# Kernel optimization log

Measured on AMD Instinct MI355X. Metric: run time of the kernel, lower is better.

## Reference

```python
import jax, jax.numpy as jnp
import numpy as np
import math

N_NODES = 100000
N_PAIRS = 640000
F_TOTAL = 128
N_HEADS = 8
HEAD_DIM = F_TOTAL // N_HEADS  # 16


def setup_inputs() -> dict:
    key = jax.random.key(0)
    ks = jax.random.split(key, 8)
    x = jax.random.normal(ks[0], (N_NODES, F_TOTAL), dtype=jnp.float32)
    w_ij = jax.random.normal(ks[1], (N_PAIRS, F_TOTAL), dtype=jnp.float32)
    idx_i = jax.random.randint(ks[2], (N_PAIRS,), 0, N_NODES, dtype=jnp.int32)
    idx_j = jax.random.randint(ks[3], (N_PAIRS,), 0, N_NODES, dtype=jnp.int32)
    phi_r_cut = jax.random.uniform(ks[4], (N_PAIRS,), dtype=jnp.float32)
    # per-head linear weights, nn.Linear convention: y = x @ W.T, W: (out, in)
    s = 1.0 / math.sqrt(HEAD_DIM)
    wq = jax.random.uniform(ks[5], (N_HEADS, HEAD_DIM, HEAD_DIM), jnp.float32, -s, s)
    wk = jax.random.uniform(ks[6], (N_HEADS, HEAD_DIM, HEAD_DIM), jnp.float32, -s, s)
    wv = jax.random.uniform(ks[7], (N_HEADS, HEAD_DIM, HEAD_DIM), jnp.float32, -s, s)
    return {"x": x, "w_ij": w_ij, "idx_i": idx_i, "idx_j": idx_j,
            "phi_r_cut": phi_r_cut, "wq": wq, "wk": wk, "wv": wv}


def reference(x, w_ij, idx_i, idx_j, phi_r_cut, wq, wk, wv):
    n, f = x.shape
    h, d = wq.shape[0], wq.shape[1]
    # split into heads: (H, n, d) and (H, P, d)
    xh = x.reshape(n, h, d).transpose(1, 0, 2)
    wh = w_ij.reshape(-1, h, d).transpose(1, 0, 2)
    # per-head linear projections (y = x @ W.T)
    q = jnp.einsum('hnd,hed->hne', xh, wq)  # (H, n, d)
    k = jnp.einsum('hnd,hed->hne', xh, wk)
    v = jnp.einsum('hnd,hed->hne', xh, wv)
    # filter-modulated dot-product attention coefficients per pair
    alpha = (q[:, idx_i] * wh * k[:, idx_j]).sum(-1) / math.sqrt(d)  # (H, P)
    alpha = alpha * phi_r_cut[None, :]
    # message + scatter-add aggregation
    msg = alpha[..., None] * v[:, idx_j]  # (H, P, d)
    y = jax.vmap(lambda m: jax.ops.segment_sum(m, idx_i, num_segments=n))(msg)  # (H, n, d)
    return y.transpose(1, 0, 2).reshape(n, f)
```

## Files before the change

### kernel.cpp

```cpp
#include <hip/hip_runtime.h>
#include <hip/hip_fp16.h>

#define F_TOTAL 128
#define N_HEADS 8
#define HEAD_DIM 16
#define SCAN_ITEMS 1024

typedef float vf4 __attribute__((ext_vector_type(4)));
typedef int   vi4 __attribute__((ext_vector_type(4)));

__global__ __launch_bounds__(256) void proj_hist_kernel(
    const float* __restrict__ x,
    const float* __restrict__ wq,
    const float* __restrict__ wk,
    const float* __restrict__ wv,
    const int*   __restrict__ idx_i,
    float* __restrict__ q, __half2* __restrict__ kv,
    int*   __restrict__ hist,
    int n_nodes, int n_pairs)
{
    const int gid = blockIdx.x * 256 + threadIdx.x;
    const int stride = gridDim.x * 256;
    const int f = gid & (F_TOTAL - 1);

    float rq[16], rk[16], rv[16];
    const float4* wq4 = (const float4*)wq;
    const float4* wk4 = (const float4*)wk;
    const float4* wv4 = (const float4*)wv;
    #pragma unroll
    for (int d4 = 0; d4 < 4; ++d4) {
        float4 a = wq4[f * 4 + d4];
        rq[d4*4+0]=a.x; rq[d4*4+1]=a.y; rq[d4*4+2]=a.z; rq[d4*4+3]=a.w;
        float4 b = wk4[f * 4 + d4];
        rk[d4*4+0]=b.x; rk[d4*4+1]=b.y; rk[d4*4+2]=b.z; rk[d4*4+3]=b.w;
        float4 c = wv4[f * 4 + d4];
        rv[d4*4+0]=c.x; rv[d4*4+1]=c.y; rv[d4*4+2]=c.z; rv[d4*4+3]=c.w;
    }
    const int lanebase = (f & 112) & 63;

    const int total = n_nodes * F_TOTAL;
    for (int idx = gid; idx < total; idx += stride) {
        const float xval = __builtin_nontemporal_load(x + idx);
        float aq = 0.f, ak = 0.f, av = 0.f;
        #pragma unroll
        for (int d = 0; d < 16; ++d) {
            const float xv = __shfl(xval, lanebase + d);
            aq += xv * rq[d];
            ak += xv * rk[d];
            av += xv * rv[d];
        }
        q[idx] = aq;
        kv[idx] = __floats2half2_rn(ak, av);
    }

    for (int p = gid; p < n_pairs; p += stride)
        atomicAdd(&hist[idx_i[p]], 1);
}

__global__ __launch_bounds__(256) void scan_reduce_kernel(
    const int* __restrict__ hist, int* __restrict__ blockSums, int n)
{
    __shared__ int ls[256];
    const int t = threadIdx.x;
    const int base = blockIdx.x * SCAN_ITEMS + t * 4;
    int s = 0;
    if (base + 3 < n) {
        int4 h = *(const int4*)(hist + base);
        s = h.x + h.y + h.z + h.w;
    } else {
        for (int kk = 0; kk < 4; ++kk)
            if (base + kk < n) s += hist[base + kk];
    }
    ls[t] = s;
    __syncthreads();
    for (int off = 128; off > 0; off >>= 1) {
        if (t < off) ls[t] += ls[t + off];
        __syncthreads();
    }
    if (t == 0) blockSums[blockIdx.x] = ls[0];
}

__global__ __launch_bounds__(256) void scan_apply_kernel(
    const int* __restrict__ hist, const int* __restrict__ blockSums,
    int* __restrict__ offsets, int n, int nblk)
{
    __shared__ int ls[256];
    const int t = threadIdx.x;
    const int bid = blockIdx.x;

    int s = 0;
    for (int b = t; b < bid; b += 256) s += blockSums[b];
    ls[t] = s;
    __syncthreads();
    for (int off = 128; off > 0; off >>= 1) {
        if (t < off) ls[t] += ls[t + off];
        __syncthreads();
    }
    const int base0 = ls[0];
    __syncthreads();

    const int base = bid * SCAN_ITEMS + t * 4;
    int h0 = 0, h1 = 0, h2 = 0, h3 = 0;
    if (base + 3 < n) {
        int4 h = *(const int4*)(hist + base);
        h0 = h.x; h1 = h.y; h2 = h.z; h3 = h.w;
    } else {
        if (base + 0 < n) h0 = hist[base + 0];
        if (base + 1 < n) h1 = hist[base + 1];
        if (base + 2 < n) h2 = hist[base + 2];
        if (base + 3 < n) h3 = hist[base + 3];
    }
    const int tsum = h0 + h1 + h2 + h3;
    ls[t] = tsum;
    __syncthreads();
    for (int off = 1; off < 256; off <<= 1) {
        int add = (t >= off) ? ls[t - off] : 0;
        __syncthreads();
        ls[t] += add;
        __syncthreads();
    }
    int off = base0 + (ls[t] - tsum);
    if (base + 0 < n) offsets[base + 0] = off; off += h0;
    if (base + 1 < n) offsets[base + 1] = off; off += h1;
    if (base + 2 < n) offsets[base + 2] = off; off += h2;
    if (base + 3 < n) offsets[base + 3] = off;
}

__global__ __launch_bounds__(256) void scatter_kernel(
    const int* __restrict__ idx_i, const int* __restrict__ idx_j,
    const float* __restrict__ phi,
    int* __restrict__ offsets,
    vi4* __restrict__ meta,
    int n_pairs)
{
    const int p = blockIdx.x * 256 + threadIdx.x;
    if (p < n_pairs) {
        const int i = idx_i[p];
        const int pos = atomicAdd(&offsets[i], 1);
        meta[pos] = (vi4){p, idx_j[p], __float_as_int(phi[p]), 0};
    }
}

__global__ __launch_bounds__(256) void segment_kernel(
    const float* __restrict__ q,
    const __half2* __restrict__ kv,
    const float* __restrict__ w_ij,
    const int* __restrict__ hist,
    const int* __restrict__ offsets,
    const vi4* __restrict__ meta,
    float* __restrict__ out,
    int n_nodes)
{
    const int node = blockIdx.x * 4 + (threadIdx.x >> 6);
    if (node >= n_nodes) return;
    const int lane = threadIdx.x & 63;
    const int half = lane >> 5;
    const int t    = lane & 31;

    const int cnt   = hist[node];
    const int start = offsets[node] - cnt;
    const vf4 q4 = *((const vf4*)(q + (size_t)node * F_TOTAL) + t);

    vf4 acc = (vf4){0.f, 0.f, 0.f, 0.f};

    const int my0 = start + half;
    const int rem = (cnt > half) ? ((cnt - half + 1) >> 1) : 0;

    union HU { vi4 i; __half2 h[4]; };

    if (rem > 0) {
        vi4 m0 = meta[my0];
        vi4 m1 = meta[my0 + 2];
        int r = 0;
        for (; r + 2 <= rem; r += 2) {
            const vi4 n0 = meta[my0 + 2 * (r + 2)];
            const vi4 n1 = meta[my0 + 2 * (r + 3)];
            const vf4 wA = __builtin_nontemporal_load(
                (const vf4*)(w_ij + (size_t)m0.x * F_TOTAL) + t);
            HU A; A.i = *((const vi4*)kv + (size_t)m0.y * 32 + t);
            const vf4 wB = __builtin_nontemporal_load(
                (const vf4*)(w_ij + (size_t)m1.x * F_TOTAL) + t);
            HU B; B.i = *((const vi4*)kv + (size_t)m1.y * 32 + t);

            const float2 a0 = __half22float2(A.h[0]);
            const float2 a1 = __half22float2(A.h[1]);
            const float2 a2 = __half22float2(A.h[2]);
            const float2 a3 = __half22float2(A.h[3]);
            const float2 b0 = __half22float2(B.h[0]);
            const float2 b1 = __half22float2(B.h[1]);
            const float2 b2 = __half22float2(B.h[2]);
            const float2 b3 = __half22float2(B.h[3]);

            float sA = q4.x*wA.x*a0.x + q4.y*wA.y*a1.x + q4.z*wA.z*a2.x + q4.w*wA.w*a3.x;
            float sB = q4.x*wB.x*b0.x + q4.y*wB.y*b1.x + q4.z*wB.z*b2.x + q4.w*wB.w*b3.x;
            sA += __shfl_xor(sA, 1); sA += __shfl_xor(sA, 2);
            sB += __shfl_xor(sB, 1); sB += __shfl_xor(sB, 2);
            const float alA = sA * 0.25f * __int_as_float(m0.z);
            const float alB = sB * 0.25f * __int_as_float(m1.z);
            acc.x += alA * a0.y; acc.y += alA * a1.y;
            acc.z += alA * a2.y; acc.w += alA * a3.y;
            acc.x += alB * b0.y; acc.y += alB * b1.y;
            acc.z += alB * b2.y; acc.w += alB * b3.y;
            m0 = n0; m1 = n1;
        }
        if (r < rem) {
            const vf4 wA = __builtin_nontemporal_load(
                (const vf4*)(w_ij + (size_t)m0.x * F_TOTAL) + t);
            HU A; A.i = *((const vi4*)kv + (size_t)m0.y * 32 + t);
            const float2 a0 = __half22float2(A.h[0]);
            const float2 a1 = __half22float2(A.h[1]);
            const float2 a2 = __half22float2(A.h[2]);
            const float2 a3 = __half22float2(A.h[3]);
            float sA = q4.x*wA.x*a0.x + q4.y*wA.y*a1.x + q4.z*wA.z*a2.x + q4.w*wA.w*a3.x;
            sA += __shfl_xor(sA, 1); sA += __shfl_xor(sA, 2);
            const float alA = sA * 0.25f * __int_as_float(m0.z);
            acc.x += alA * a0.y; acc.y += alA * a1.y;
            acc.z += alA * a2.y; acc.w += alA * a3.y;
        }
    }

    acc.x += __shfl_xor(acc.x, 32);
    acc.y += __shfl_xor(acc.y, 32);
    acc.z += __shfl_xor(acc.z, 32);
    acc.w += __shfl_xor(acc.w, 32);
    if (half == 0)
        __builtin_nontemporal_store(acc, (vf4*)(out + (size_t)node * F_TOTAL) + t);
}

extern "C" void kernel_launch(void* const* d_in, const int* in_sizes, int n_in,
                              void* d_out, int out_size, void* d_ws, size_t ws_size,
                              hipStream_t stream)
{
    const float* x     = (const float*)d_in[0];
    const float* w_ij  = (const float*)d_in[1];
    const int*   idx_i = (const int*)d_in[2];
    const int*   idx_j = (const int*)d_in[3];
    const float* phi   = (const float*)d_in[4];
    const float* wq    = (const float*)d_in[5];
    const float* wk    = (const float*)d_in[6];
    const float* wv    = (const float*)d_in[7];

    const int n_nodes = in_sizes[0] / F_TOTAL;
    const int n_pairs = in_sizes[2];
    const size_t node_elems = (size_t)n_nodes * F_TOTAL;

    float*   q         = (float*)d_ws;
    __half2* kv        = (__half2*)(q + node_elems);
    vi4*     meta      = (vi4*)((char*)kv + node_elems * sizeof(__half2));
    int*     hist      = (int*)(meta + n_pairs + 8);
    int*     offsets   = hist + n_nodes;
    int*     blockSums = offsets + n_nodes;

    hipMemsetAsync(hist, 0, (size_t)n_nodes * sizeof(int), stream);

    proj_hist_kernel<<<3072, 256, 0, stream>>>(
        x, wq, wk, wv, idx_i, q, kv, hist, n_nodes, n_pairs);

    const int nblk = (n_nodes + SCAN_ITEMS - 1) / SCAN_ITEMS;
    scan_reduce_kernel<<<nblk, 256, 0, stream>>>(hist, blockSums, n_nodes);
    scan_apply_kernel<<<nblk, 256, 0, stream>>>(hist, blockSums, offsets,
                                                n_nodes, nblk);

    const int pair_blocks = (n_pairs + 255) / 256;
    scatter_kernel<<<pair_blocks, 256, 0, stream>>>(
        idx_i, idx_j, phi, offsets, meta, n_pairs);

    segment_kernel<<<(n_nodes + 3) / 4, 256, 0, stream>>>(
        q, kv, w_ij, hist, offsets, meta, (float*)d_out, n_nodes);
}
```

Measured before the change: 590.8 us.

## Pre-sort w_ij into destination order as fp16 during scatter

```diff
diff --git a/kernel.cpp b/kernel.cpp
--- a/kernel.cpp
+++ b/kernel.cpp
@@ -129,25 +129,43 @@
 __global__ __launch_bounds__(256) void scatter_kernel(
     const int* __restrict__ idx_i, const int* __restrict__ idx_j,
     const float* __restrict__ phi,
+    const float* __restrict__ w_ij,
     int* __restrict__ offsets,
-    vi4* __restrict__ meta,
+    int2* __restrict__ meta,
+    __half* __restrict__ w16s,
     int n_pairs)
 {
-    const int p = blockIdx.x * 256 + threadIdx.x;
-    if (p < n_pairs) {
-        const int i = idx_i[p];
-        const int pos = atomicAdd(&offsets[i], 1);
-        meta[pos] = (vi4){p, idx_j[p], __float_as_int(phi[p]), 0};
-    }
+    const int grp = (blockIdx.x * 256 + threadIdx.x) >> 4;
+    const int l16 = threadIdx.x & 15;
+    const int lane = threadIdx.x & 63;
+    if (grp >= n_pairs) return;
+
+    int pos = 0;
+    if (l16 == 0) pos = atomicAdd(&offsets[idx_i[grp]], 1);
+    pos = __shfl(pos, lane & 48);
+
+    const vf4 wa = __builtin_nontemporal_load(
+        (const vf4*)(w_ij + (size_t)grp * F_TOTAL) + l16 * 2);
+    const vf4 wb = __builtin_nontemporal_load(
+        (const vf4*)(w_ij + (size_t)grp * F_TOTAL) + l16 * 2 + 1);
+    union { vi4 i; __half2 h[4]; } o;
+    o.h[0] = __floats2half2_rn(wa.x, wa.y);
+    o.h[1] = __floats2half2_rn(wa.z, wa.w);
+    o.h[2] = __floats2half2_rn(wb.x, wb.y);
+    o.h[3] = __floats2half2_rn(wb.z, wb.w);
+    *((vi4*)w16s + (size_t)pos * 16 + l16) = o.i;
+
+    if (l16 == 0)
+        meta[pos] = (int2){idx_j[grp], __float_as_int(phi[grp])};
 }
 
 __global__ __launch_bounds__(256) void segment_kernel(
     const float* __restrict__ q,
     const __half2* __restrict__ kv,
-    const float* __restrict__ w_ij,
+    const __half* __restrict__ w16s,
     const int* __restrict__ hist,
     const int* __restrict__ offsets,
-    const vi4* __restrict__ meta,
+    const int2* __restrict__ meta,
     float* __restrict__ out,
     int n_nodes)
 {
@@ -167,21 +185,24 @@
     const int rem = (cnt > half) ? ((cnt - half + 1) >> 1) : 0;
 
     union HU { vi4 i; __half2 h[4]; };
+    union WU { int2 i2; __half2 h[2]; };
 
     if (rem > 0) {
-        vi4 m0 = meta[my0];
-        vi4 m1 = meta[my0 + 2];
+        int2 m0 = meta[my0];
+        int2 m1 = meta[my0 + 2];
         int r = 0;
         for (; r + 2 <= rem; r += 2) {
-            const vi4 n0 = meta[my0 + 2 * (r + 2)];
-            const vi4 n1 = meta[my0 + 2 * (r + 3)];
-            const vf4 wA = __builtin_nontemporal_load(
-                (const vf4*)(w_ij + (size_t)m0.x * F_TOTAL) + t);
-            HU A; A.i = *((const vi4*)kv + (size_t)m0.y * 32 + t);
-            const vf4 wB = __builtin_nontemporal_load(
-                (const vf4*)(w_ij + (size_t)m1.x * F_TOTAL) + t);
-            HU B; B.i = *((const vi4*)kv + (size_t)m1.y * 32 + t);
-
+            const int2 n0 = meta[my0 + 2 * (r + 2)];
+            const int2 n1 = meta[my0 + 2 * (r + 3)];
+            WU wA; wA.i2 = *(const int2*)(w16s + (size_t)(my0 + 2*r)     * F_TOTAL + t * 4);
+            HU A;  A.i   = *((const vi4*)kv + (size_t)m0.x * 32 + t);
+            WU wB; wB.i2 = *(const int2*)(w16s + (size_t)(my0 + 2*(r+1)) * F_TOTAL + t * 4);
+            HU B;  B.i   = *((const vi4*)kv + (size_t)m1.x * 32 + t);
+
+            const float2 wa0 = __half22float2(wA.h[0]);
+            const float2 wa1 = __half22float2(wA.h[1]);
+            const float2 wb0 = __half22float2(wB.h[0]);
+            const float2 wb1 = __half22float2(wB.h[1]);
             const float2 a0 = __half22float2(A.h[0]);
             const float2 a1 = __half22float2(A.h[1]);
             const float2 a2 = __half22float2(A.h[2]);
@@ -191,12 +212,12 @@
             const float2 b2 = __half22float2(B.h[2]);
             const float2 b3 = __half22float2(B.h[3]);
 
-            float sA = q4.x*wA.x*a0.x + q4.y*wA.y*a1.x + q4.z*wA.z*a2.x + q4.w*wA.w*a3.x;
-            float sB = q4.x*wB.x*b0.x + q4.y*wB.y*b1.x + q4.z*wB.z*b2.x + q4.w*wB.w*b3.x;
+            float sA = q4.x*wa0.x*a0.x + q4.y*wa0.y*a1.x + q4.z*wa1.x*a2.x + q4.w*wa1.y*a3.x;
+            float sB = q4.x*wb0.x*b0.x + q4.y*wb0.y*b1.x + q4.z*wb1.x*b2.x + q4.w*wb1.y*b3.x;
             sA += __shfl_xor(sA, 1); sA += __shfl_xor(sA, 2);
             sB += __shfl_xor(sB, 1); sB += __shfl_xor(sB, 2);
-            const float alA = sA * 0.25f * __int_as_float(m0.z);
-            const float alB = sB * 0.25f * __int_as_float(m1.z);
+            const float alA = sA * 0.25f * __int_as_float(m0.y);
+            const float alB = sB * 0.25f * __int_as_float(m1.y);
             acc.x += alA * a0.y; acc.y += alA * a1.y;
             acc.z += alA * a2.y; acc.w += alA * a3.y;
             acc.x += alB * b0.y; acc.y += alB * b1.y;
@@ -204,16 +225,17 @@
             m0 = n0; m1 = n1;
         }
         if (r < rem) {
-            const vf4 wA = __builtin_nontemporal_load(
-                (const vf4*)(w_ij + (size_t)m0.x * F_TOTAL) + t);
-            HU A; A.i = *((const vi4*)kv + (size_t)m0.y * 32 + t);
+            WU wA; wA.i2 = *(const int2*)(w16s + (size_t)(my0 + 2*r) * F_TOTAL + t * 4);
+            HU A;  A.i   = *((const vi4*)kv + (size_t)m0.x * 32 + t);
+            const float2 wa0 = __half22float2(wA.h[0]);
+            const float2 wa1 = __half22float2(wA.h[1]);
             const float2 a0 = __half22float2(A.h[0]);
             const float2 a1 = __half22float2(A.h[1]);
             const float2 a2 = __half22float2(A.h[2]);
             const float2 a3 = __half22float2(A.h[3]);
-            float sA = q4.x*wA.x*a0.x + q4.y*wA.y*a1.x + q4.z*wA.z*a2.x + q4.w*wA.w*a3.x;
+            float sA = q4.x*wa0.x*a0.x + q4.y*wa0.y*a1.x + q4.z*wa1.x*a2.x + q4.w*wa1.y*a3.x;
             sA += __shfl_xor(sA, 1); sA += __shfl_xor(sA, 2);
-            const float alA = sA * 0.25f * __int_as_float(m0.z);
+            const float alA = sA * 0.25f * __int_as_float(m0.y);
             acc.x += alA * a0.y; acc.y += alA * a1.y;
             acc.z += alA * a2.y; acc.w += alA * a3.y;
         }
@@ -246,7 +268,8 @@
 
     float*   q         = (float*)d_ws;
     __half2* kv        = (__half2*)(q + node_elems);
-    vi4*     meta      = (vi4*)((char*)kv + node_elems * sizeof(__half2));
+    __half*  w16s      = (__half*)(kv + node_elems);
+    int2*    meta      = (int2*)(w16s + (size_t)(n_pairs + 1) * F_TOTAL);
     int*     hist      = (int*)(meta + n_pairs + 8);
     int*     offsets   = hist + n_nodes;
     int*     blockSums = offsets + n_nodes;
@@ -261,10 +284,10 @@
     scan_apply_kernel<<<nblk, 256, 0, stream>>>(hist, blockSums, offsets,
                                                 n_nodes, nblk);
 
-    const int pair_blocks = (n_pairs + 255) / 256;
-    scatter_kernel<<<pair_blocks, 256, 0, stream>>>(
-        idx_i, idx_j, phi, offsets, meta, n_pairs);
+    const int scat_blocks = (n_pairs * 16 + 255) / 256;
+    scatter_kernel<<<scat_blocks, 256, 0, stream>>>(
+        idx_i, idx_j, phi, w_ij, offsets, meta, w16s, n_pairs);
 
     segment_kernel<<<(n_nodes + 3) / 4, 256, 0, stream>>>(
-        q, kv, w_ij, hist, offsets, meta, (float*)d_out, n_nodes);
-}
+        q, kv, w16s, hist, offsets, meta, (float*)d_out, n_nodes);
+}
```

After: 644.0 us. 1.09x slower.
